# Kernel tuning notes

Measured on AMD Instinct MI355X. Metric: run time of the kernel, lower is better.

## Reference

```python
import jax, jax.numpy as jnp
import numpy as np

EPS = 1e-6


def setup_inputs() -> dict:
    key = jax.random.key(0)
    k1, k2 = jax.random.split(key)
    B, Lq, Lk, D = 16, 1024, 1024, 512
    query = jax.random.normal(k1, (B, Lq, D), dtype=jnp.float32)
    context = jax.random.normal(k2, (B, Lk, D), dtype=jnp.float32)
    gamma = jnp.ones((D,), dtype=jnp.float32)
    beta = jnp.zeros((D,), dtype=jnp.float32)
    return {"query": query, "context": context, "gamma": gamma, "beta": beta}


def _layer_norm(x, gamma, beta):
    mean = jnp.mean(x, axis=-1, keepdims=True)
    var = jnp.var(x, axis=-1, keepdims=True)
    return gamma * (x - mean) * jax.lax.rsqrt(var + EPS) + beta


def reference(query, context, gamma, beta):
    # query: [B, Lq, D], context: [B, Lk, D]
    D = query.shape[-1]
    scale = 1.0 / np.sqrt(D).astype(np.float32)
    # additive-style tanh-activated scores: [B, Lq, Lk]
    score = jnp.tanh(jnp.einsum('bqd,bkd->bqk', query, context) * scale)
    attn = jax.nn.softmax(score, axis=2)
    # dropout is identity in eval/reference mode
    out = jnp.einsum('bqk,bkd->bqd', attn, context)
    out = _layer_norm(out + query, gamma, beta)
    return out
```

## Files before the change

### kernel.cpp

```cpp
#include <hip/hip_runtime.h>
#include <hip/hip_bf16.h>
#include <cstdint>

#define LQ 1024
#define LK 1024
#define DD 512
#define NB 16
#define QB 64
#define KB 32
#define NT (LK / KB)
#define CSTRIDE 1088

typedef short bf16x8 __attribute__((ext_vector_type(8)));
typedef float f32x4 __attribute__((ext_vector_type(4)));

__device__ __forceinline__ uint16_t f2bf(float f) {
  uint32_t u = __builtin_bit_cast(uint32_t, f);
  u = (u + 0x7fffu + ((u >> 16) & 1u)) >> 16;
  return (uint16_t)u;
}

__device__ __forceinline__ void load_lds16(const void* g, void* l) {
  __builtin_amdgcn_global_load_lds(
      (const __attribute__((address_space(1))) uint32_t*)g,
      (__attribute__((address_space(3))) uint32_t*)l, 16, 0, 0);
}

__global__ __launch_bounds__(256) void prep_kernel(const float* __restrict__ c,
                                                   uint16_t* __restrict__ cb,
                                                   uint16_t* __restrict__ ct) {
  __shared__ float t[32][33];
  const int k0 = blockIdx.x * 32, d0 = blockIdx.y * 32, b = blockIdx.z;
  const float* src = c + (size_t)b * LK * DD;
  uint16_t* cbd = cb + (size_t)b * LK * DD;
  uint16_t* ctd = ct + (size_t)b * DD * LK;
  const int tx = threadIdx.x, ty = threadIdx.y;
  for (int j = 0; j < 4; ++j) {
    int k = ty + j * 8;
    float v = src[(size_t)(k0 + k) * DD + d0 + tx];
    t[k][tx] = v;
    cbd[(size_t)(k0 + k) * DD + d0 + tx] = f2bf(v);
  }
  __syncthreads();
  for (int j = 0; j < 4; ++j) {
    int d = ty + j * 8;
    ctd[(size_t)(d0 + d) * LK + k0 + tx] = f2bf(t[tx][d]);
  }
}

__global__ __launch_bounds__(512, 2) void attn_kernel(
    const uint16_t* __restrict__ Cb, const uint16_t* __restrict__ Ctb,
    const float* __restrict__ Qf, const float* __restrict__ gamma,
    const float* __restrict__ beta, float* __restrict__ out) {
  __shared__ uint4 cs4[2][32 * CSTRIDE / 16];
  __shared__ char plds[2][64 * 80];
  __shared__ float denom_s[64];
  __shared__ float rsum_s[64], rsumsq_s[64], mean_s[64], rstd_s[64];

  const int tid = threadIdx.x;
  const int w = tid >> 6, l = tid & 63, c = l & 15, g = l >> 4;
  const int orig = blockIdx.x;
  const int virt = ((orig & 7) << 5) | (orig >> 3);
  const int b = virt >> 4, qblk = virt & 15;
  const int q0 = qblk * QB;
  const int mt = w & 1, qt = w >> 1;
  const float scale = 0.044194173824159216f;

  if (tid < 64) { denom_s[tid] = 0.f; rsum_s[tid] = 0.f; rsumsq_s[tid] = 0.f; }

  bf16x8 qfrag[16];
  {
    const float* qrow = Qf + ((size_t)b * LQ + q0 + qt * 16 + c) * DD;
    for (int s = 0; s < 16; ++s) {
      float4 a0 = *(const float4*)(qrow + s * 32 + g * 8);
      float4 a1 = *(const float4*)(qrow + s * 32 + g * 8 + 4);
      ushort4 u0, u1;
      u0.x = f2bf(a0.x); u0.y = f2bf(a0.y); u0.z = f2bf(a0.z); u0.w = f2bf(a0.w);
      u1.x = f2bf(a1.x); u1.y = f2bf(a1.y); u1.z = f2bf(a1.z); u1.w = f2bf(a1.w);
      union { ushort4 u[2]; bf16x8 v; } pk;
      pk.u[0] = u0; pk.u[1] = u1;
      qfrag[s] = pk.v;
    }
  }

  const int kkA = mt * 16 + c;
  const char* arow0 = (const char*)cs4[0] + kkA * CSTRIDE + ((g ^ (kkA & 3)) * 16);
  const char* arow1 = (const char*)cs4[1] + kkA * CSTRIDE + ((g ^ (kkA & 3)) * 16);

  f32x4 oacc[4][4];
  for (int i = 0; i < 4; ++i)
    for (int j = 0; j < 4; ++j) oacc[i][j] = (f32x4){0.f, 0.f, 0.f, 0.f};
  float dacc = 0.f;

  const char* cbyte = (const char*)Cb + (size_t)b * LK * DD * 2;
  const char* ctbyte = (const char*)Ctb + (size_t)b * DD * LK * 2;

  int csrcoff[4];
  for (int j = 0; j < 4; ++j) {
    int r = w * 4 + j;
    csrcoff[j] = r * 1024 + ((l * 16) ^ ((r & 3) << 4));
  }
  const char* pbbase = ctbyte + (size_t)(w * 64 + c) * 2048 + g * 16;

  char* pwr0 = plds[0] + (qt * 16 + c) * 80 + (mt * 16 + g * 4) * 2;
  char* pwr1 = plds[1] + (qt * 16 + c) * 80 + (mt * 16 + g * 4) * 2;
  const char* par0 = plds[0] + c * 80 + g * 16;
  const char* par1 = plds[1] + c * 80 + g * 16;

  auto stageC = [&](int buf, int kt2) {
    const char* s0 = cbyte + (size_t)kt2 * 32768;
    char* base = (char*)cs4[buf];
    for (int j = 0; j < 4; ++j)
      load_lds16(s0 + csrcoff[j], base + (w * 4 + j) * CSTRIDE);
  };
  auto loadPB = [&](bf16x8(&pbn)[4], int kt2) {
    const char* p = pbbase + kt2 * 64;
    pbn[0] = *(const bf16x8*)(p);
    pbn[1] = *(const bf16x8*)(p + 32768);
    pbn[2] = *(const bf16x8*)(p + 65536);
    pbn[3] = *(const bf16x8*)(p + 98304);
  };

  bf16x8 pbA[4], pbB[4];

  stageC(0, 0);
  __syncthreads();

  auto body = [&](int kt, bf16x8(&pbc)[4], bf16x8(&pbn)[4]) {
    const int cur = kt & 1;
    if (kt + 1 < NT) stageC(cur ^ 1, kt + 1);
    loadPB(pbn, kt);
    if (kt) {
      const char* par = cur ? par0 : par1;
      bf16x8 pa[4];
      for (int q2 = 0; q2 < 4; ++q2) pa[q2] = *(const bf16x8*)(par + q2 * 1280);
      __builtin_amdgcn_s_setprio(1);
      for (int q2 = 0; q2 < 4; ++q2)
        for (int n2 = 0; n2 < 4; ++n2)
          oacc[q2][n2] =
              __builtin_amdgcn_mfma_f32_16x16x32_bf16(pa[q2], pbc[n2], oacc[q2][n2], 0, 0, 0);
      __builtin_amdgcn_s_setprio(0);
    }
    f32x4 sacc = {0.f, 0.f, 0.f, 0.f};
    {
      const char* arow = cur ? arow1 : arow0;
      __builtin_amdgcn_s_setprio(1);
      for (int s = 0; s < 16; ++s) {
        bf16x8 a = *(const bf16x8*)(arow + s * 64);
        sacc = __builtin_amdgcn_mfma_f32_16x16x32_bf16(a, qfrag[s], sacc, 0, 0, 0);
      }
      __builtin_amdgcn_s_setprio(0);
    }
    {
      float pv[4];
      for (int i = 0; i < 4; ++i) {
        float sv = sacc[i] * scale;
        float e2 = __expf(sv * 2.f);
        float r = __builtin_amdgcn_rcpf(e2 + 1.f);
        float th = (e2 - 1.f) * r;
        float p = __expf(th);
        pv[i] = p;
        dacc += p;
      }
      uint2 pk;
      pk.x = ((uint32_t)f2bf(pv[1]) << 16) | f2bf(pv[0]);
      pk.y = ((uint32_t)f2bf(pv[3]) << 16) | f2bf(pv[2]);
      *(uint2*)(cur ? pwr1 : pwr0) = pk;
    }
    __syncthreads();
  };

  for (int kt = 0; kt < NT; kt += 2) {
    body(kt, pbB, pbA);
    body(kt + 1, pbA, pbB);
  }
  {
    bf16x8 pa[4];
    for (int q2 = 0; q2 < 4; ++q2) pa[q2] = *(const bf16x8*)(par1 + q2 * 1280);
    for (int q2 = 0; q2 < 4; ++q2)
      for (int n2 = 0; n2 < 4; ++n2)
        oacc[q2][n2] =
            __builtin_amdgcn_mfma_f32_16x16x32_bf16(pa[q2], pbB[n2], oacc[q2][n2], 0, 0, 0);
  }

  float dv = dacc;
  dv += __shfl_xor(dv, 16);
  dv += __shfl_xor(dv, 32);
  if (l < 16) atomicAdd(&denom_s[qt * 16 + l], dv);
  __syncthreads();

  const float* qsrc = Qf + ((size_t)b * LQ + q0) * DD;
  for (int q2 = 0; q2 < 4; ++q2)
    for (int i = 0; i < 4; ++i) {
      int row = q2 * 16 + g * 4 + i;
      float inv = 1.f / denom_s[row];
      for (int nt = 0; nt < 4; ++nt) {
        int d = w * 64 + nt * 16 + c;
        float o = oacc[q2][nt][i] * inv + qsrc[(size_t)row * DD + d];
        oacc[q2][nt][i] = o;
      }
    }
  for (int q2 = 0; q2 < 4; ++q2)
    for (int i = 0; i < 4; ++i) {
      float s1 = 0.f, s2 = 0.f;
      for (int nt = 0; nt < 4; ++nt) {
        float v = oacc[q2][nt][i];
        s1 += v;
        s2 += v * v;
      }
      s1 += __shfl_xor(s1, 1); s2 += __shfl_xor(s2, 1);
      s1 += __shfl_xor(s1, 2); s2 += __shfl_xor(s2, 2);
      s1 += __shfl_xor(s1, 4); s2 += __shfl_xor(s2, 4);
      s1 += __shfl_xor(s1, 8); s2 += __shfl_xor(s2, 8);
      if (c == 0) {
        int row = q2 * 16 + g * 4 + i;
        atomicAdd(&rsum_s[row], s1);
        atomicAdd(&rsumsq_s[row], s2);
      }
    }
  __syncthreads();
  if (tid < 64) {
    float m = rsum_s[tid] * (1.f / DD);
    float var = rsumsq_s[tid] * (1.f / DD) - m * m;
    mean_s[tid] = m;
    rstd_s[tid] = rsqrtf(fmaxf(var, 0.f) + 1e-6f);
  }
  __syncthreads();
  float* op = out + ((size_t)b * LQ + q0) * DD;
  for (int q2 = 0; q2 < 4; ++q2)
    for (int i = 0; i < 4; ++i) {
      int row = q2 * 16 + g * 4 + i;
      float m = mean_s[row], r = rstd_s[row];
      for (int nt = 0; nt < 4; ++nt) {
        int d = w * 64 + nt * 16 + c;
        op[(size_t)row * DD + d] = gamma[d] * ((oacc[q2][nt][i] - m) * r) + beta[d];
      }
    }
}

__global__ __launch_bounds__(256) void naive_kernel(const float* __restrict__ Q,
                                                    const float* __restrict__ C,
                                                    const float* __restrict__ gamma,
                                                    const float* __restrict__ beta,
                                                    float* __restrict__ out) {
  const int row = blockIdx.x;
  const int b = row >> 10;
  const int tid = threadIdx.x;
  __shared__ float qs[DD];
  __shared__ float ps[LK];
  __shared__ float ys[DD];
  __shared__ float red[256];
  const float* qp = Q + (size_t)row * DD;
  const float* cb = C + (size_t)b * LK * DD;
  for (int d = tid; d < DD; d += 256) qs[d] = qp[d];
  __syncthreads();
  for (int k = tid; k < LK; k += 256) {
    const float* cr = cb + (size_t)k * DD;
    float s = 0.f;
    for (int d = 0; d < DD; ++d) s += qs[d] * cr[d];
    s *= 0.044194173824159216f;
    float e2 = __expf(2.f * s);
    float th = (e2 - 1.f) / (e2 + 1.f);
    ps[k] = __expf(th);
  }
  __syncthreads();
  float dsum = 0.f;
  for (int k = tid; k < LK; k += 256) dsum += ps[k];
  red[tid] = dsum;
  __syncthreads();
  for (int off = 128; off; off >>= 1) {
    if (tid < off) red[tid] += red[tid + off];
    __syncthreads();
  }
  float inv = 1.f / red[0];
  __syncthreads();
  for (int d = tid; d < DD; d += 256) {
    float o = 0.f;
    for (int k = 0; k < LK; ++k) o += ps[k] * cb[(size_t)k * DD + d];
    ys[d] = o * inv + qs[d];
  }
  __syncthreads();
  float s1 = 0.f;
  for (int d = tid; d < DD; d += 256) s1 += ys[d];
  red[tid] = s1;
  __syncthreads();
  for (int off = 128; off; off >>= 1) {
    if (tid < off) red[tid] += red[tid + off];
    __syncthreads();
  }
  float mean = red[0] * (1.f / DD);
  __syncthreads();
  float s2 = 0.f;
  for (int d = tid; d < DD; d += 256) {
    float v = ys[d] - mean;
    s2 += v * v;
  }
  red[tid] = s2;
  __syncthreads();
  for (int off = 128; off; off >>= 1) {
    if (tid < off) red[tid] += red[tid + off];
    __syncthreads();
  }
  float rstd = rsqrtf(red[0] * (1.f / DD) + 1e-6f);
  for (int d = tid; d < DD; d += 256)
    out[(size_t)row * DD + d] = gamma[d] * ((ys[d] - mean) * rstd) + beta[d];
}

extern "C" void kernel_launch(void* const* d_in, const int* in_sizes, int n_in,
                              void* d_out, int out_size, void* d_ws, size_t ws_size,
                              hipStream_t stream) {
  const float* Qf = (const float*)d_in[0];
  const float* Cf = (const float*)d_in[1];
  const float* gamma = (const float*)d_in[2];
  const float* beta = (const float*)d_in[3];
  float* out = (float*)d_out;
  const size_t nelem = (size_t)NB * LK * DD;
  const size_t need = nelem * 2 * 2;
  if (ws_size >= need) {
    uint16_t* Cb = (uint16_t*)d_ws;
    uint16_t* Ctb = Cb + nelem;
    prep_kernel<<<dim3(LK / 32, DD / 32, NB), dim3(32, 8), 0, stream>>>(Cf, Cb, Ctb);
    attn_kernel<<<256, 512, 0, stream>>>(Cb, Ctb, Qf, gamma, beta, out);
  } else {
    naive_kernel<<<NB * LQ, 256, 0, stream>>>(Qf, Cf, gamma, beta, out);
  }
}
```

Measured before the change: 95.72 us.

## Triple-buffer context and P tiles, prefetch two ahead, split score accumulators

The LDS staging of context tiles and of probability tiles moves from double to triple buffering, and the context load now prefetches two iterations ahead so global-to-LDS latency has more time to hide. The score MFMA chain is split into two independent accumulators to shorten the dependency chain. The full __syncthreads is replaced by an LDS-count wait plus a raw barrier and a sched_barrier. This raises LDS use to about 120KB per block, and it relies on the register loads' vmcnt waits to cover the async LDS loads.

```diff
diff --git a/kernel.cpp b/kernel.cpp
--- a/kernel.cpp
+++ b/kernel.cpp
@@ -10,6 +10,8 @@
 #define KB 32
 #define NT (LK / KB)
 #define CSTRIDE 1088
+#define CSZ (32 * CSTRIDE)
+#define PSZ (64 * 80)
 
 typedef short bf16x8 __attribute__((ext_vector_type(8)));
 typedef float f32x4 __attribute__((ext_vector_type(4)));
@@ -52,8 +54,8 @@
     const uint16_t* __restrict__ Cb, const uint16_t* __restrict__ Ctb,
     const float* __restrict__ Qf, const float* __restrict__ gamma,
     const float* __restrict__ beta, float* __restrict__ out) {
-  __shared__ uint4 cs4[2][32 * CSTRIDE / 16];
-  __shared__ char plds[2][64 * 80];
+  __shared__ uint4 cs4[3 * CSZ / 16];
+  __shared__ char plds[3 * PSZ];
   __shared__ float denom_s[64];
   __shared__ float rsum_s[64], rsumsq_s[64], mean_s[64], rstd_s[64];
 
@@ -84,8 +86,7 @@
   }
 
   const int kkA = mt * 16 + c;
-  const char* arow0 = (const char*)cs4[0] + kkA * CSTRIDE + ((g ^ (kkA & 3)) * 16);
-  const char* arow1 = (const char*)cs4[1] + kkA * CSTRIDE + ((g ^ (kkA & 3)) * 16);
+  const int aoff = kkA * CSTRIDE + ((g ^ (kkA & 3)) * 16);
 
   f32x4 oacc[4][4];
   for (int i = 0; i < 4; ++i)
@@ -102,16 +103,19 @@
   }
   const char* pbbase = ctbyte + (size_t)(w * 64 + c) * 2048 + g * 16;
 
-  char* pwr0 = plds[0] + (qt * 16 + c) * 80 + (mt * 16 + g * 4) * 2;
-  char* pwr1 = plds[1] + (qt * 16 + c) * 80 + (mt * 16 + g * 4) * 2;
-  const char* par0 = plds[0] + c * 80 + g * 16;
-  const char* par1 = plds[1] + c * 80 + g * 16;
-
-  auto stageC = [&](int buf, int kt2) {
+  char* cs0 = (char*)cs4;
+  char* cs1 = cs0 + CSZ;
+  char* cs2 = cs1 + CSZ;
+  char* pl0 = plds;
+  char* pl1 = pl0 + PSZ;
+  char* pl2 = pl1 + PSZ;
+  const int pwoff = (qt * 16 + c) * 80 + (mt * 16 + g * 4) * 2;
+  const int proff = c * 80 + g * 16;
+
+  auto stageC = [&](char* dst, int kt2) {
     const char* s0 = cbyte + (size_t)kt2 * 32768;
-    char* base = (char*)cs4[buf];
     for (int j = 0; j < 4; ++j)
-      load_lds16(s0 + csrcoff[j], base + (w * 4 + j) * CSTRIDE);
+      load_lds16(s0 + csrcoff[j], dst + (w * 4 + j) * CSTRIDE);
   };
   auto loadPB = [&](bf16x8(&pbn)[4], int kt2) {
     const char* p = pbbase + kt2 * 64;
@@ -121,19 +125,19 @@
     pbn[3] = *(const bf16x8*)(p + 98304);
   };
 
-  bf16x8 pbA[4], pbB[4];
-
-  stageC(0, 0);
-  __syncthreads();
-
-  auto body = [&](int kt, bf16x8(&pbc)[4], bf16x8(&pbn)[4]) {
-    const int cur = kt & 1;
-    if (kt + 1 < NT) stageC(cur ^ 1, kt + 1);
+  bf16x8 pbX[4], pbY[4], pbZ[4];
+
+  stageC(cs0, 0);
+  stageC(cs1, 1);
+  __syncthreads();
+
+  auto body = [&](int kt, const char* csR, char* csW, const char* pR, char* pW,
+                  bf16x8(&pbc)[4], bf16x8(&pbn)[4], bool doStage, bool doPV) {
+    if (doStage) stageC(csW, kt + 2);
     loadPB(pbn, kt);
-    if (kt) {
-      const char* par = cur ? par0 : par1;
+    if (doPV) {
       bf16x8 pa[4];
-      for (int q2 = 0; q2 < 4; ++q2) pa[q2] = *(const bf16x8*)(par + q2 * 1280);
+      for (int q2 = 0; q2 < 4; ++q2) pa[q2] = *(const bf16x8*)(pR + proff + q2 * 1280);
       __builtin_amdgcn_s_setprio(1);
       for (int q2 = 0; q2 < 4; ++q2)
         for (int n2 = 0; n2 < 4; ++n2)
@@ -141,20 +145,22 @@
               __builtin_amdgcn_mfma_f32_16x16x32_bf16(pa[q2], pbc[n2], oacc[q2][n2], 0, 0, 0);
       __builtin_amdgcn_s_setprio(0);
     }
-    f32x4 sacc = {0.f, 0.f, 0.f, 0.f};
+    f32x4 s0v = {0.f, 0.f, 0.f, 0.f}, s1v = {0.f, 0.f, 0.f, 0.f};
     {
-      const char* arow = cur ? arow1 : arow0;
+      const char* ar = csR + aoff;
       __builtin_amdgcn_s_setprio(1);
-      for (int s = 0; s < 16; ++s) {
-        bf16x8 a = *(const bf16x8*)(arow + s * 64);
-        sacc = __builtin_amdgcn_mfma_f32_16x16x32_bf16(a, qfrag[s], sacc, 0, 0, 0);
+      for (int s = 0; s < 8; ++s) {
+        bf16x8 a0 = *(const bf16x8*)(ar + s * 64);
+        bf16x8 a1 = *(const bf16x8*)(ar + (s + 8) * 64);
+        s0v = __builtin_amdgcn_mfma_f32_16x16x32_bf16(a0, qfrag[s], s0v, 0, 0, 0);
+        s1v = __builtin_amdgcn_mfma_f32_16x16x32_bf16(a1, qfrag[s + 8], s1v, 0, 0, 0);
       }
       __builtin_amdgcn_s_setprio(0);
     }
     {
       float pv[4];
       for (int i = 0; i < 4; ++i) {
-        float sv = sacc[i] * scale;
+        float sv = (s0v[i] + s1v[i]) * scale;
         float e2 = __expf(sv * 2.f);
         float r = __builtin_amdgcn_rcpf(e2 + 1.f);
         float th = (e2 - 1.f) * r;
@@ -165,22 +171,27 @@
       uint2 pk;
       pk.x = ((uint32_t)f2bf(pv[1]) << 16) | f2bf(pv[0]);
       pk.y = ((uint32_t)f2bf(pv[3]) << 16) | f2bf(pv[2]);
-      *(uint2*)(cur ? pwr1 : pwr0) = pk;
-    }
-    __syncthreads();
+      *(uint2*)(pW + pwoff) = pk;
+    }
+    asm volatile("s_waitcnt lgkmcnt(0)" ::: "memory");
+    __builtin_amdgcn_s_barrier();
+    __builtin_amdgcn_sched_barrier(0);
   };
 
-  for (int kt = 0; kt < NT; kt += 2) {
-    body(kt, pbB, pbA);
-    body(kt + 1, pbA, pbB);
-  }
+  for (int kt = 0; kt < NT - 2; kt += 3) {
+    body(kt,     cs0, cs2, pl2, pl0, pbZ, pbX, kt + 2 < NT, kt > 0);
+    body(kt + 1, cs1, cs0, pl0, pl1, pbX, pbY, kt + 3 < NT, true);
+    body(kt + 2, cs2, cs1, pl1, pl2, pbY, pbZ, kt + 4 < NT, true);
+  }
+  body(NT - 2, cs0, cs2, pl2, pl0, pbZ, pbX, false, true);
+  body(NT - 1, cs1, cs0, pl0, pl1, pbX, pbY, false, true);
   {
     bf16x8 pa[4];
-    for (int q2 = 0; q2 < 4; ++q2) pa[q2] = *(const bf16x8*)(par1 + q2 * 1280);
+    for (int q2 = 0; q2 < 4; ++q2) pa[q2] = *(const bf16x8*)(pl1 + proff + q2 * 1280);
     for (int q2 = 0; q2 < 4; ++q2)
       for (int n2 = 0; n2 < 4; ++n2)
         oacc[q2][n2] =
-            __builtin_amdgcn_mfma_f32_16x16x32_bf16(pa[q2], pbB[n2], oacc[q2][n2], 0, 0, 0);
+            __builtin_amdgcn_mfma_f32_16x16x32_bf16(pa[q2], pbY[n2], oacc[q2][n2], 0, 0, 0);
   }
 
   float dv = dacc;
```

New measurement: 96.15 us. No clear change (+0.4%).
